# Kernel tuning notes

Hardware: AMD Instinct MI355X
Metric: run time of the kernel (lower is better)

Reference implementation:

```python
import jax, jax.numpy as jnp
import numpy as np

NUM_BASIS = 9  # ADVANCED_LIB in oikan: x, x^2, x^3, exp, log(|x|+1), sqrt(|x|), tanh, sin, abs


def _basis(x):
    # x: [B, Din] -> [B, Din, K] basis expansion matching ADVANCED_LIB
    ax = jnp.abs(x)
    return jnp.stack([
        x,
        x * x,
        x * x * x,
        jnp.exp(x),
        jnp.log(ax + 1.0),
        jnp.sqrt(ax),
        jnp.tanh(x),
        jnp.sin(x),
        ax,
    ], axis=-1)


def setup_inputs() -> dict:
    key = jax.random.key(0)
    k1, k2, k3 = jax.random.split(key, 3)
    B, Din, Dout, K = 4096, 128, 128, NUM_BASIS
    x = jax.random.normal(k1, (B, Din), dtype=jnp.float32)
    # per-edge basis weights (SymbolicEdge.weights ~ randn)
    W = jax.random.normal(k2, (Din, Dout, K), dtype=jnp.float32)
    # per-edge bias (initialized to zeros in SymbolicEdge)
    bias = jnp.zeros((Din, Dout), dtype=jnp.float32)
    # combination_weights ~ 0.1 * randn
    C = jax.random.normal(k3, (Din, Dout), dtype=jnp.float32) * 0.1
    return {"x": x, "W": W, "bias": bias, "C": C}


def reference(x, W, bias, C):
    feats = _basis(x)  # [B, Din, K]
    # edge_outputs[b, i, o] = sum_k feats[b,i,k] * W[i,o,k] + bias[i,o]
    edge = jnp.einsum('bik,iok->bio', feats, W) + bias  # [B, Din, Dout]
    # combined sum over input dim with combination weights
    return jnp.einsum('bio,io->bo', edge, C)  # [B, Dout]
```

## Files before the change

### kernel.cpp

```cpp
#include <hip/hip_runtime.h>
#include <math.h>


#define DIN   128
#define DOUT  128
#define NB    9
#define KK    (DIN * NB)
#define BATCH 4096

typedef __bf16 bf16x8 __attribute__((ext_vector_type(8)));
typedef float  f32x4  __attribute__((ext_vector_type(4)));

__global__ __launch_bounds__(128) void feats_kernel(const float* __restrict__ x,
                                                    __bf16* __restrict__ feats) {
    __shared__ __bf16 row[KK];
    const int b = blockIdx.x;
    const int i = threadIdx.x;
    const float v  = x[b * DIN + i];
    const float av = fabsf(v);

    float f[NB];
    f[0] = v;
    f[1] = v * v;
    f[2] = v * v * v;
    f[3] = __expf(v);
    f[4] = __logf(av + 1.0f);
    f[5] = __builtin_sqrtf(av);
    f[6] = tanhf(v);
    f[7] = __sinf(v);
    f[8] = av;

    #pragma unroll
    for (int k = 0; k < NB; ++k) row[i * NB + k] = (__bf16)f[k];
    __syncthreads();

    const unsigned int* src = (const unsigned int*)row;
    unsigned int* dst = (unsigned int*)feats + (size_t)b * (KK / 2);
    for (int j = i; j < KK / 2; j += 128) dst[j] = src[j];
}

__global__ __launch_bounds__(256) void fold_kernel(const float* __restrict__ W,
                                                   const float* __restrict__ bias,
                                                   const float* __restrict__ C,
                                                   __bf16* __restrict__ BT,
                                                   float* __restrict__ bterm) {
    const int idx = blockIdx.x * 256 + threadIdx.x;
    const int o = idx / KK;
    const int r = idx - o * KK;
    const int i = r / NB;
    const int k = r - i * NB;
    const float w = W[((size_t)i * DOUT + o) * NB + k];
    const float c = C[i * DOUT + o];
    BT[idx] = (__bf16)(w * c);

    if (blockIdx.x == 0 && threadIdx.x < DOUT) {
        const int oo = threadIdx.x;
        float s = 0.0f;
        for (int ii = 0; ii < DIN; ++ii)
            s += bias[ii * DOUT + oo] * C[ii * DOUT + oo];
        bterm[oo] = s;
    }
}

__global__ __launch_bounds__(512, 1) void gemm_kernel(const __bf16* __restrict__ A,
                                                      const __bf16* __restrict__ BT,
                                                      const float* __restrict__ bterm,
                                                      float* __restrict__ out) {
    const int lane = threadIdx.x & 63;
    const int wave = threadIdx.x >> 6;
    const int m    = lane & 15;
    const int quad = lane >> 4;
    const int row0 = blockIdx.x << 4;
    const int col0 = wave << 4;

    const bf16x8* Ap = (const bf16x8*)(A  + (size_t)(row0 + m) * KK + quad * 8);
    const bf16x8* Bp = (const bf16x8*)(BT + (size_t)(col0 + m) * KK + quad * 8);

    f32x4 acc = {0.0f, 0.0f, 0.0f, 0.0f};

    #pragma unroll 6
    for (int kc = 0; kc < KK / 32; ++kc) {
        bf16x8 a = Ap[kc * 4];
        bf16x8 b = Bp[kc * 4];
        acc = __builtin_amdgcn_mfma_f32_16x16x32_bf16(a, b, acc, 0, 0, 0);
    }

    const float bt = bterm[col0 + m];
    float* op = out + (size_t)(row0 + quad * 4) * DOUT + col0 + m;
    #pragma unroll
    for (int r = 0; r < 4; ++r) op[(size_t)r * DOUT] = acc[r] + bt;
}

extern "C" void kernel_launch(void* const* d_in, const int* in_sizes, int n_in,
                              void* d_out, int out_size, void* d_ws, size_t ws_size,
                              hipStream_t stream) {
    const float* x    = (const float*)d_in[0];
    const float* W    = (const float*)d_in[1];
    const float* bias = (const float*)d_in[2];
    const float* C    = (const float*)d_in[3];
    float* out = (float*)d_out;

    char* ws = (char*)d_ws;
    __bf16* feats = (__bf16*)ws;
    __bf16* BT    = (__bf16*)(ws + (size_t)BATCH * KK * 2);
    float*  bterm = (float*)(ws + (size_t)BATCH * KK * 2 + (size_t)DOUT * KK * 2);

    feats_kernel<<<BATCH, 128, 0, stream>>>(x, feats);
    fold_kernel<<<(DOUT * KK) / 256, 256, 0, stream>>>(W, bias, C, BT, bterm);
    gemm_kernel<<<BATCH / 16, 512, 0, stream>>>(feats, BT, bterm, out);
}
```

Before: 86.99 us.

## Fuse basis feature expansion into GEMM kernel via shared memory A tile

Removes the separate feats kernel, so basis features are no longer written to and reread from global memory as a bf16 matrix. Each GEMM block now computes its 16-row slice of features directly into padded LDS and runs the MFMA loop reading A from shared memory. This drops one launch and the intermediate global traffic. The cost is that the transcendental work sits on the GEMM's critical path, with a sync before the matmul.

```diff
diff --git a/kernel.cpp b/kernel.cpp
--- a/kernel.cpp
+++ b/kernel.cpp
@@ -7,37 +7,12 @@
 #define NB    9
 #define KK    (DIN * NB)
 #define BATCH 4096
+#define ROWS  16
+#define APAD  8
+#define ASTR  (KK + APAD)
 
 typedef __bf16 bf16x8 __attribute__((ext_vector_type(8)));
 typedef float  f32x4  __attribute__((ext_vector_type(4)));
-
-__global__ __launch_bounds__(128) void feats_kernel(const float* __restrict__ x,
-                                                    __bf16* __restrict__ feats) {
-    __shared__ __bf16 row[KK];
-    const int b = blockIdx.x;
-    const int i = threadIdx.x;
-    const float v  = x[b * DIN + i];
-    const float av = fabsf(v);
-
-    float f[NB];
-    f[0] = v;
-    f[1] = v * v;
-    f[2] = v * v * v;
-    f[3] = __expf(v);
-    f[4] = __logf(av + 1.0f);
-    f[5] = __builtin_sqrtf(av);
-    f[6] = tanhf(v);
-    f[7] = __sinf(v);
-    f[8] = av;
-
-    #pragma unroll
-    for (int k = 0; k < NB; ++k) row[i * NB + k] = (__bf16)f[k];
-    __syncthreads();
-
-    const unsigned int* src = (const unsigned int*)row;
-    unsigned int* dst = (unsigned int*)feats + (size_t)b * (KK / 2);
-    for (int j = i; j < KK / 2; j += 128) dst[j] = src[j];
-}
 
 __global__ __launch_bounds__(256) void fold_kernel(const float* __restrict__ W,
                                                    const float* __restrict__ bias,
@@ -62,26 +37,50 @@
     }
 }
 
-__global__ __launch_bounds__(512, 1) void gemm_kernel(const __bf16* __restrict__ A,
-                                                      const __bf16* __restrict__ BT,
-                                                      const float* __restrict__ bterm,
-                                                      float* __restrict__ out) {
-    const int lane = threadIdx.x & 63;
-    const int wave = threadIdx.x >> 6;
+__global__ __launch_bounds__(512, 1) void fused_kernel(const float* __restrict__ x,
+                                                       const __bf16* __restrict__ BT,
+                                                       const float* __restrict__ bterm,
+                                                       float* __restrict__ out) {
+    __shared__ __bf16 As[ROWS * ASTR];
+    const int t    = threadIdx.x;
+    const int row0 = blockIdx.x * ROWS;
+
+    for (int e = t; e < ROWS * DIN; e += 512) {
+        const int r = e >> 7;
+        const int i = e & 127;
+        const float v  = x[(size_t)(row0 + r) * DIN + i];
+        const float av = fabsf(v);
+        float f[NB];
+        f[0] = v;
+        f[1] = v * v;
+        f[2] = v * v * v;
+        f[3] = __expf(v);
+        f[4] = __logf(av + 1.0f);
+        f[5] = __builtin_sqrtf(av);
+        f[6] = tanhf(v);
+        f[7] = __sinf(v);
+        f[8] = av;
+        __bf16* dst = &As[r * ASTR + i * NB];
+        #pragma unroll
+        for (int k = 0; k < NB; ++k) dst[k] = (__bf16)f[k];
+    }
+    __syncthreads();
+
+    const int lane = t & 63;
+    const int wave = t >> 6;
     const int m    = lane & 15;
     const int quad = lane >> 4;
-    const int row0 = blockIdx.x << 4;
     const int col0 = wave << 4;
 
-    const bf16x8* Ap = (const bf16x8*)(A  + (size_t)(row0 + m) * KK + quad * 8);
-    const bf16x8* Bp = (const bf16x8*)(BT + (size_t)(col0 + m) * KK + quad * 8);
+    const __bf16* Ap = &As[m * ASTR + quad * 8];
+    const __bf16* Bp = BT + (size_t)(col0 + m) * KK + quad * 8;
 
     f32x4 acc = {0.0f, 0.0f, 0.0f, 0.0f};
 
     #pragma unroll 6
     for (int kc = 0; kc < KK / 32; ++kc) {
-        bf16x8 a = Ap[kc * 4];
-        bf16x8 b = Bp[kc * 4];
+        bf16x8 a = *(const bf16x8*)(Ap + kc * 32);
+        bf16x8 b = *(const bf16x8*)(Bp + kc * 32);
         acc = __builtin_amdgcn_mfma_f32_16x16x32_bf16(a, b, acc, 0, 0, 0);
     }
 
@@ -101,11 +100,9 @@
     float* out = (float*)d_out;
 
     char* ws = (char*)d_ws;
-    __bf16* feats = (__bf16*)ws;
-    __bf16* BT    = (__bf16*)(ws + (size_t)BATCH * KK * 2);
-    float*  bterm = (float*)(ws + (size_t)BATCH * KK * 2 + (size_t)DOUT * KK * 2);
+    __bf16* BT    = (__bf16*)ws;
+    float*  bterm = (float*)(ws + (size_t)DOUT * KK * 2);
 
-    feats_kernel<<<BATCH, 128, 0, stream>>>(x, feats);
     fold_kernel<<<(DOUT * KK) / 256, 256, 0, stream>>>(W, bias, C, BT, bterm);
-    gemm_kernel<<<BATCH / 16, 512, 0, stream>>>(feats, BT, bterm, out);
+    fused_kernel<<<BATCH / ROWS, 512, 0, stream>>>(x, BT, bterm, out);
 }
```

Result: faster. 74.51 us (-14.3%).
